# Performance work log

Hardware: AMD Instinct MI355X
Metric: run time of the kernel (lower is better)

The kernel has to match this reference:

```python
import jax, jax.numpy as jnp
import numpy as np

BATCH_SIZE = 4096
D = 128
TEMPERATURE = 0.5
EPS = 1e-8  # torch CosineSimilarity eps


def _neg_indices(batch_size):
    # flat indices of the (N, N-2) negative entries: all but diagonal and the +/-B pair
    N = 2 * batch_size
    mask = np.ones((N, N), dtype=bool)
    np.fill_diagonal(mask, False)
    i = np.arange(batch_size)
    mask[i, batch_size + i] = False
    mask[batch_size + i, i] = False
    return np.where(mask.ravel())[0]


NEG_IDX = jnp.asarray(_neg_indices(BATCH_SIZE))


def setup_inputs() -> dict:
    key = jax.random.key(0)
    k1, k2 = jax.random.split(key)
    return {
        "z_i": jax.random.normal(k1, (BATCH_SIZE, D), dtype=jnp.float32),
        "z_j": jax.random.normal(k2, (BATCH_SIZE, D), dtype=jnp.float32),
    }


def reference(z_i, z_j):
    batch_size = z_i.shape[0]
    N = 2 * batch_size
    z = jnp.concatenate([z_i, z_j], axis=0)                       # [N, D]
    norm = jnp.maximum(jnp.linalg.norm(z, axis=1, keepdims=True), EPS)
    zn = z / norm
    sim = (zn @ zn.T) / TEMPERATURE                               # [N, N] cosine sim / temp
    # positives: diagonals at offset +/- batch_size
    pos = jnp.concatenate(
        [jnp.diagonal(sim, offset=batch_size), jnp.diagonal(sim, offset=-batch_size)],
        axis=0,
    )                                                             # [N]
    neg = sim.ravel()[NEG_IDX].reshape(N, N - 2)                  # masked gather
    logits = jnp.concatenate([pos[:, None], neg], axis=1)         # [N, N-1], label = 0
    # CrossEntropyLoss(reduction='sum') with labels all 0, then / N
    loss = jnp.sum(jax.nn.logsumexp(logits, axis=1) - logits[:, 0]) / N
    return loss
```

## Files before the change

### kernel.cpp

```cpp
#include <hip/hip_runtime.h>
#include <hip/hip_bf16.h>


#define BATCH 4096
#define N_TOT 8192
#define DIM 128
#define GRP 128
#define NGRP 64
#define TILE_C 64
#define NTASK 2080

#define C_LOG2E2 2.8853900817779268f

using bf16x8 = __attribute__((ext_vector_type(8))) __bf16;
using f32x4  = __attribute__((ext_vector_type(4))) float;

typedef __attribute__((address_space(1))) const void cg_void;
typedef __attribute__((address_space(3))) void lds_void;
__device__ __forceinline__ void gll16(const void* g, void* l) {
    __builtin_amdgcn_global_load_lds((cg_void*)g, (lds_void*)l, 16, 0, 0);
}

__global__ __launch_bounds__(256) void k_normalize(const float* __restrict__ zi,
                                                   const float* __restrict__ zj,
                                                   __hip_bfloat16* __restrict__ zn) {
    int row  = blockIdx.x * 4 + (threadIdx.x >> 6);
    int lane = threadIdx.x & 63;
    const float* src = (row < BATCH) ? (zi + (size_t)row * DIM)
                                     : (zj + (size_t)(row - BATCH) * DIM);
    float2 v = ((const float2*)src)[lane];
    float ss = v.x * v.x + v.y * v.y;
    #pragma unroll
    for (int m = 1; m < 64; m <<= 1) ss += __shfl_xor(ss, m);
    float inv = 1.0f / fmaxf(sqrtf(ss), 1e-8f);
    __hip_bfloat162 o;
    o.x = __float2bfloat16(v.x * inv);
    o.y = __float2bfloat16(v.y * inv);
    ((__hip_bfloat162*)(zn + (size_t)row * DIM))[lane] = o;
}

__global__ __launch_bounds__(256, 3) void k_main(const __hip_bfloat16* __restrict__ zn_,
                                                 float* __restrict__ S_contrib) {
    __shared__ __align__(16) char Bs[2][TILE_C * 256];
    __shared__ float colred[4][GRP];

    const int tid  = threadIdx.x;
    const int lane = tid & 63;
    const int wv   = tid >> 6;
    const int l15  = lane & 15;
    const int lb   = lane >> 4;

    const int idx = blockIdx.x;
    int I = (int)(64.5f - sqrtf(64.5f * 64.5f - 2.0f * (float)idx));
    int base = 64 * I - ((I * (I - 1)) >> 1);
    if (idx < base)                 { --I; base = 64 * I - ((I * (I - 1)) >> 1); }
    else if (idx >= base + 64 - I)  { ++I; base = 64 * I - ((I * (I - 1)) >> 1); }
    const int J = I + (idx - base);
    const bool isdiag = (I == J);

    const int wr0 = I * GRP + wv * 32;

    const __bf16* zn = (const __bf16*)zn_;

    bf16x8 a_[2][4];
    #pragma unroll
    for (int g = 0; g < 2; ++g) {
        const __bf16* p = zn + (size_t)(wr0 + g * 16 + l15) * DIM + lb * 8;
        #pragma unroll
        for (int s = 0; s < 4; ++s)
            a_[g][s] = *(const bf16x8*)(p + s * 32);
    }

    const char* gB = (const char*)(zn + (size_t)J * GRP * DIM);
    {
        int srcoff[4];
        #pragma unroll
        for (int i = 0; i < 4; ++i) {
            int m2 = (wv * 4 + i) * 64 + lane;
            int col = m2 >> 4, slot = m2 & 15;
            srcoff[i] = col * 256 + (slot ^ (col & 7)) * 16;
        }
        #pragma unroll
        for (int t = 0; t < 2; ++t) {
            const char* src = gB + (size_t)t * (TILE_C * 256);
            #pragma unroll
            for (int i = 0; i < 4; ++i)
                gll16(src + srcoff[i], Bs[t] + (wv * 4 + i) * 1024);
        }
    }

    f32x4 sumexp[2] = {};

    __syncthreads();

    auto CMP = [&](int t) {
        const char* buf = Bs[t];
        const int c0t = J * GRP + t * TILE_C;
        const bool diagtile = ((unsigned)(wr0 - c0t) < (unsigned)TILE_C);
        float csr4[4];
        #pragma unroll
        for (int cb = 0; cb < 4; ++cb) {
            const int cc = cb * 16 + l15;
            const char* pc = buf + cc * 256;
            bf16x8 b[4];
            #pragma unroll
            for (int s = 0; s < 4; ++s)
                b[s] = *(const bf16x8*)(pc + ((lb + s * 4) ^ (cc & 7)) * 16);
            f32x4 acc[2] = {};
            #pragma unroll
            for (int g = 0; g < 2; ++g)
                #pragma unroll
                for (int s = 0; s < 4; ++s)
                    acc[g] = __builtin_amdgcn_mfma_f32_16x16x32_bf16(a_[g][s], b[s], acc[g], 0, 0, 0);
            const int mycol = c0t + cc;
            if (diagtile) {
                #pragma unroll
                for (int g = 0; g < 2; ++g)
                    #pragma unroll
                    for (int v = 0; v < 4; ++v) {
                        float e = __builtin_amdgcn_exp2f(acc[g][v] * C_LOG2E2);
                        int row = wr0 + g * 16 + lb * 4 + v;
                        sumexp[g][v] += (mycol == row) ? 0.0f : e;
                    }
                csr4[cb] = 0.0f;
            } else {
                float cs = 0.0f;
                #pragma unroll
                for (int g = 0; g < 2; ++g)
                    #pragma unroll
                    for (int v = 0; v < 4; ++v) {
                        float e = __builtin_amdgcn_exp2f(acc[g][v] * C_LOG2E2);
                        sumexp[g][v] += e;
                        cs += e;
                    }
                csr4[cb] = cs;
            }
        }
        if (!isdiag) {
            #pragma unroll
            for (int cb = 0; cb < 4; ++cb) {
                float v = csr4[cb];
                v += __shfl_xor(v, 16);
                v += __shfl_xor(v, 32);
                if (lb == 0) colred[wv][t * TILE_C + cb * 16 + l15] = v;
            }
        }
    };

    CMP(0);
    CMP(1);

    #pragma unroll
    for (int m = 1; m <= 8; m <<= 1)
        #pragma unroll
        for (int g = 0; g < 2; ++g)
            #pragma unroll
            for (int v = 0; v < 4; ++v)
                sumexp[g][v] += __shfl_xor(sumexp[g][v], m);

    if (l15 == 0) {
        #pragma unroll
        for (int g = 0; g < 2; ++g) {
            int row = wr0 + g * 16 + lb * 4;
            *(f32x4*)&S_contrib[(size_t)J * N_TOT + row] = sumexp[g];
        }
    }

    if (!isdiag) {
        __syncthreads();
        if (tid < GRP) {
            float s = colred[0][tid] + colred[1][tid] + colred[2][tid] + colred[3][tid];
            S_contrib[(size_t)I * N_TOT + J * GRP + tid] = s;
        }
    }
}

__device__ inline float bdot(unsigned a, unsigned b) {
    float alo = __uint_as_float(a << 16), ahi = __uint_as_float(a & 0xffff0000u);
    float blo = __uint_as_float(b << 16), bhi = __uint_as_float(b & 0xffff0000u);
    return fmaf(alo, blo, ahi * bhi);
}

__global__ __launch_bounds__(256) void k_rowsum(const float* __restrict__ S_contrib,
                                                const __hip_bfloat16* __restrict__ zn_,
                                                float* __restrict__ blk_out) {
    const int r = blockIdx.x * 256 + threadIdx.x;
    float S = 0.0f;
    #pragma unroll
    for (int s = 0; s < NGRP; ++s) S += S_contrib[(size_t)s * N_TOT + r];

    const uint4* pa = (const uint4*)((const __bf16*)zn_ + (size_t)r * DIM);
    const uint4* pb = (const uint4*)((const __bf16*)zn_ + (size_t)(r ^ BATCH) * DIM);
    float dot = 0.0f;
    #pragma unroll
    for (int cc = 0; cc < DIM / 8; ++cc) {
        uint4 ua = pa[cc], ub = pb[cc];
        dot += bdot(ua.x, ub.x) + bdot(ua.y, ub.y) + bdot(ua.z, ub.z) + bdot(ua.w, ub.w);
    }

    float contrib = __logf(S) - 2.0f * dot;

    #pragma unroll
    for (int m = 1; m < 64; m <<= 1) contrib += __shfl_xor(contrib, m);
    __shared__ float sm[4];
    if ((threadIdx.x & 63) == 0) sm[threadIdx.x >> 6] = contrib;
    __syncthreads();
    if (threadIdx.x == 0) blk_out[blockIdx.x] = sm[0] + sm[1] + sm[2] + sm[3];
}

__global__ void k_final(const float* __restrict__ blk_out, float* __restrict__ out) {
    float v = (threadIdx.x < 32) ? blk_out[threadIdx.x] : 0.0f;
    #pragma unroll
    for (int m = 1; m < 64; m <<= 1) v += __shfl_xor(v, m);
    if (threadIdx.x == 0) out[0] = v / (float)N_TOT;
}

extern "C" void kernel_launch(void* const* d_in, const int* in_sizes, int n_in,
                              void* d_out, int out_size, void* d_ws, size_t ws_size,
                              hipStream_t stream) {
    const float* zi = (const float*)d_in[0];
    const float* zj = (const float*)d_in[1];
    char* ws = (char*)d_ws;
    __hip_bfloat16* zn = (__hip_bfloat16*)ws;
    float* S_contrib = (float*)(ws + (size_t)2 * 1024 * 1024);
    float* blk       = (float*)(ws + (size_t)4 * 1024 * 1024);
    float* out       = (float*)d_out;

    k_normalize<<<N_TOT / 4, 256, 0, stream>>>(zi, zj, zn);
    k_main<<<NTASK, 256, 0, stream>>>(zn, S_contrib);
    k_rowsum<<<N_TOT / 256, 256, 0, stream>>>(S_contrib, zn, blk);
    k_final<<<1, 64, 0, stream>>>(blk, out);
}
```

Before: 37.16 us.

## Fuse final reduction via ticket, reuse MFMA positives, alias colred onto LDS

Several changes land at once. The separate k_final launch is replaced by a last-block-done atomic ticket inside k_rowsum, and the ticket is reset in k_normalize. Positive-pair logits are written out of the MFMA accumulators in the J==I+32 tiles instead of being recomputed as bf16 dot products in k_rowsum. The colred LDS array now aliases the B tile buffer, which needs an extra barrier, and MFMA sections get s_setprio while k_normalize uses a grid-stride loop with fewer blocks. The aim is to cut one launch, the dot-product work and LDS footprint, at the cost of an extra sync and atomics.

```diff
diff --git a/kernel.cpp b/kernel.cpp
--- a/kernel.cpp
+++ b/kernel.cpp
@@ -23,27 +23,31 @@
 
 __global__ __launch_bounds__(256) void k_normalize(const float* __restrict__ zi,
                                                    const float* __restrict__ zj,
-                                                   __hip_bfloat16* __restrict__ zn) {
-    int row  = blockIdx.x * 4 + (threadIdx.x >> 6);
+                                                   __hip_bfloat16* __restrict__ zn,
+                                                   int* __restrict__ ticket) {
+    if (blockIdx.x == 0 && threadIdx.x == 0) *ticket = 0;
     int lane = threadIdx.x & 63;
-    const float* src = (row < BATCH) ? (zi + (size_t)row * DIM)
-                                     : (zj + (size_t)(row - BATCH) * DIM);
-    float2 v = ((const float2*)src)[lane];
-    float ss = v.x * v.x + v.y * v.y;
-    #pragma unroll
-    for (int m = 1; m < 64; m <<= 1) ss += __shfl_xor(ss, m);
-    float inv = 1.0f / fmaxf(sqrtf(ss), 1e-8f);
-    __hip_bfloat162 o;
-    o.x = __float2bfloat16(v.x * inv);
-    o.y = __float2bfloat16(v.y * inv);
-    ((__hip_bfloat162*)(zn + (size_t)row * DIM))[lane] = o;
+    int wv   = threadIdx.x >> 6;
+    for (int row = blockIdx.x * 4 + wv; row < N_TOT; row += 512 * 4) {
+        const float* src = (row < BATCH) ? (zi + (size_t)row * DIM)
+                                         : (zj + (size_t)(row - BATCH) * DIM);
+        float2 v = ((const float2*)src)[lane];
+        float ss = v.x * v.x + v.y * v.y;
+        #pragma unroll
+        for (int m = 1; m < 64; m <<= 1) ss += __shfl_xor(ss, m);
+        float inv = 1.0f / fmaxf(sqrtf(ss), 1e-8f);
+        __hip_bfloat162 o;
+        o.x = __float2bfloat16(v.x * inv);
+        o.y = __float2bfloat16(v.y * inv);
+        ((__hip_bfloat162*)(zn + (size_t)row * DIM))[lane] = o;
+    }
 }
 
 __global__ __launch_bounds__(256, 3) void k_main(const __hip_bfloat16* __restrict__ zn_,
-                                                 float* __restrict__ S_contrib) {
+                                                 float* __restrict__ S_contrib,
+                                                 float* __restrict__ pos) {
     __shared__ __align__(16) char Bs[2][TILE_C * 256];
-    __shared__ float colred[4][GRP];
-
+    float* colred = (float*)Bs;
     const int tid  = threadIdx.x;
     const int lane = tid & 63;
     const int wv   = tid >> 6;
@@ -57,6 +61,7 @@
     else if (idx >= base + 64 - I)  { ++I; base = 64 * I - ((I * (I - 1)) >> 1); }
     const int J = I + (idx - base);
     const bool isdiag = (I == J);
+    const bool haspos = (J == I + 32);
 
     const int wr0 = I * GRP + wv * 32;
 
@@ -90,6 +95,7 @@
     }
 
     f32x4 sumexp[2] = {};
+    float csr[2][4];
 
     __syncthreads();
 
@@ -97,7 +103,6 @@
         const char* buf = Bs[t];
         const int c0t = J * GRP + t * TILE_C;
         const bool diagtile = ((unsigned)(wr0 - c0t) < (unsigned)TILE_C);
-        float csr4[4];
         #pragma unroll
         for (int cb = 0; cb < 4; ++cb) {
             const int cc = cb * 16 + l15;
@@ -107,12 +112,23 @@
             for (int s = 0; s < 4; ++s)
                 b[s] = *(const bf16x8*)(pc + ((lb + s * 4) ^ (cc & 7)) * 16);
             f32x4 acc[2] = {};
+            __builtin_amdgcn_s_setprio(1);
             #pragma unroll
             for (int g = 0; g < 2; ++g)
                 #pragma unroll
                 for (int s = 0; s < 4; ++s)
                     acc[g] = __builtin_amdgcn_mfma_f32_16x16x32_bf16(a_[g][s], b[s], acc[g], 0, 0, 0);
+            __builtin_amdgcn_s_setprio(0);
             const int mycol = c0t + cc;
+            if (haspos) {
+                #pragma unroll
+                for (int g = 0; g < 2; ++g)
+                    #pragma unroll
+                    for (int v = 0; v < 4; ++v) {
+                        int row = wr0 + g * 16 + lb * 4 + v;
+                        if (mycol == row + BATCH) pos[row] = acc[g][v];
+                    }
+            }
             if (diagtile) {
                 #pragma unroll
                 for (int g = 0; g < 2; ++g)
@@ -122,7 +138,7 @@
                         int row = wr0 + g * 16 + lb * 4 + v;
                         sumexp[g][v] += (mycol == row) ? 0.0f : e;
                     }
-                csr4[cb] = 0.0f;
+                csr[t][cb] = 0.0f;
             } else {
                 float cs = 0.0f;
                 #pragma unroll
@@ -133,16 +149,7 @@
                         sumexp[g][v] += e;
                         cs += e;
                     }
-                csr4[cb] = cs;
-            }
-        }
-        if (!isdiag) {
-            #pragma unroll
-            for (int cb = 0; cb < 4; ++cb) {
-                float v = csr4[cb];
-                v += __shfl_xor(v, 16);
-                v += __shfl_xor(v, 32);
-                if (lb == 0) colred[wv][t * TILE_C + cb * 16 + l15] = v;
+                csr[t][cb] = cs;
             }
         }
     };
@@ -168,51 +175,57 @@
 
     if (!isdiag) {
         __syncthreads();
+        #pragma unroll
+        for (int t = 0; t < 2; ++t)
+            #pragma unroll
+            for (int cb = 0; cb < 4; ++cb) {
+                float v = csr[t][cb];
+                v += __shfl_xor(v, 16);
+                v += __shfl_xor(v, 32);
+                if (lb == 0) colred[wv * GRP + t * TILE_C + cb * 16 + l15] = v;
+            }
+        __syncthreads();
         if (tid < GRP) {
-            float s = colred[0][tid] + colred[1][tid] + colred[2][tid] + colred[3][tid];
+            float s = colred[0 * GRP + tid] + colred[1 * GRP + tid]
+                    + colred[2 * GRP + tid] + colred[3 * GRP + tid];
             S_contrib[(size_t)I * N_TOT + J * GRP + tid] = s;
         }
     }
 }
 
-__device__ inline float bdot(unsigned a, unsigned b) {
-    float alo = __uint_as_float(a << 16), ahi = __uint_as_float(a & 0xffff0000u);
-    float blo = __uint_as_float(b << 16), bhi = __uint_as_float(b & 0xffff0000u);
-    return fmaf(alo, blo, ahi * bhi);
-}
-
 __global__ __launch_bounds__(256) void k_rowsum(const float* __restrict__ S_contrib,
-                                                const __hip_bfloat16* __restrict__ zn_,
-                                                float* __restrict__ blk_out) {
+                                                const float* __restrict__ pos,
+                                                float* __restrict__ blk,
+                                                int* __restrict__ ticket,
+                                                float* __restrict__ out) {
     const int r = blockIdx.x * 256 + threadIdx.x;
     float S = 0.0f;
     #pragma unroll
     for (int s = 0; s < NGRP; ++s) S += S_contrib[(size_t)s * N_TOT + r];
 
-    const uint4* pa = (const uint4*)((const __bf16*)zn_ + (size_t)r * DIM);
-    const uint4* pb = (const uint4*)((const __bf16*)zn_ + (size_t)(r ^ BATCH) * DIM);
-    float dot = 0.0f;
-    #pragma unroll
-    for (int cc = 0; cc < DIM / 8; ++cc) {
-        uint4 ua = pa[cc], ub = pb[cc];
-        dot += bdot(ua.x, ub.x) + bdot(ua.y, ub.y) + bdot(ua.z, ub.z) + bdot(ua.w, ub.w);
-    }
-
-    float contrib = __logf(S) - 2.0f * dot;
+    float contrib = __logf(S) - 2.0f * pos[r & (BATCH - 1)];
 
     #pragma unroll
     for (int m = 1; m < 64; m <<= 1) contrib += __shfl_xor(contrib, m);
     __shared__ float sm[4];
+    __shared__ int winner;
     if ((threadIdx.x & 63) == 0) sm[threadIdx.x >> 6] = contrib;
     __syncthreads();
-    if (threadIdx.x == 0) blk_out[blockIdx.x] = sm[0] + sm[1] + sm[2] + sm[3];
-}
-
-__global__ void k_final(const float* __restrict__ blk_out, float* __restrict__ out) {
-    float v = (threadIdx.x < 32) ? blk_out[threadIdx.x] : 0.0f;
-    #pragma unroll
-    for (int m = 1; m < 64; m <<= 1) v += __shfl_xor(v, m);
-    if (threadIdx.x == 0) out[0] = v / (float)N_TOT;
+    if (threadIdx.x == 0) {
+        blk[blockIdx.x] = sm[0] + sm[1] + sm[2] + sm[3];
+        __threadfence();
+        winner = (atomicAdd(ticket, 1) == 31);
+    }
+    __syncthreads();
+    if (winner) {
+        __threadfence();
+        if (threadIdx.x < 32) {
+            float v = blk[threadIdx.x];
+            #pragma unroll
+            for (int m = 1; m < 32; m <<= 1) v += __shfl_xor(v, m);
+            if (threadIdx.x == 0) out[0] = v / (float)N_TOT;
+        }
+    }
 }
 
 extern "C" void kernel_launch(void* const* d_in, const int* in_sizes, int n_in,
@@ -224,10 +237,11 @@
     __hip_bfloat16* zn = (__hip_bfloat16*)ws;
     float* S_contrib = (float*)(ws + (size_t)2 * 1024 * 1024);
     float* blk       = (float*)(ws + (size_t)4 * 1024 * 1024);
+    int*   ticket    = (int*)  (ws + (size_t)4 * 1024 * 1024 + 128);
+    float* pos       = (float*)(ws + (size_t)4 * 1024 * 1024 + 256);
     float* out       = (float*)d_out;
 
-    k_normalize<<<N_TOT / 4, 256, 0, stream>>>(zi, zj, zn);
-    k_main<<<NTASK, 256, 0, stream>>>(zn, S_contrib);
-    k_rowsum<<<N_TOT / 256, 256, 0, stream>>>(S_contrib, zn, blk);
-    k_final<<<1, 64, 0, stream>>>(blk, out);
-}
+    k_normalize<<<512, 256, 0, stream>>>(zi, zj, zn, ticket);
+    k_main<<<NTASK, 256, 0, stream>>>(zn, S_contrib, pos);
+    k_rowsum<<<N_TOT / 256, 256, 0, stream>>>(S_contrib, pos, blk, ticket, out);
+}
```

New measurement: 49.70 us. +33.7%, slower.
